# Kernel tuning notes

Measured on AMD Instinct MI355X. Metric: run time of the kernel, lower is better.

Reference implementation:

```python
import jax, jax.numpy as jnp
import numpy as np
from jax import lax

N_ITER = 50  # SparsemaxBisectFunction hardcodes n_iter=50


def _sparsemax_bisect(X):
    # alpha = 2: gp(x)=x, gp_inv(y)=y, p(x)=clamp(x, 0). X*(alpha-1) == X.
    d = X.shape[-1]
    max_val = jnp.max(X, axis=-1, keepdims=True)
    tau_lo = max_val - 1.0          # max - gp(1)
    tau_hi = max_val - 1.0 / d      # max - gp(1/d)
    f_lo = jnp.sum(jnp.maximum(X - tau_lo, 0.0), axis=-1) - 1.0
    dm = tau_hi - tau_lo

    def body(_, carry):
        tau_lo, dm, _tau_m = carry
        dm = dm * 0.5
        tau_m = tau_lo + dm
        f_m = jnp.sum(jnp.maximum(X - tau_m, 0.0), axis=-1) - 1.0
        mask = (f_m * f_lo >= 0.0)[..., None]
        tau_lo = jnp.where(mask, tau_m, tau_lo)
        return tau_lo, dm, tau_m

    _, _, tau_m = lax.fori_loop(0, N_ITER, body, (tau_lo, dm, tau_lo))
    p = jnp.maximum(X - tau_m, 0.0)  # p_m from the last bisection iteration
    p = p / jnp.sum(p, axis=-1, keepdims=True)  # ensure_sum_one=True
    return p


def setup_inputs() -> dict:
    key = jax.random.key(0)
    X = jax.random.normal(key, (4096, 32000), dtype=jnp.float32)
    return {"X": X}


def reference(X):
    return _sparsemax_bisect(X)
```

## Files before the change

### kernel.cpp

```cpp
#include <hip/hip_runtime.h>
#include <math.h>
#include <stdint.h>

constexpr int D = 32000;
constexpr int BLOCK = 1024;
constexpr int NW = BLOCK / 64;
constexpr int FULL4 = D / (4 * BLOCK);
constexpr int REM_THREADS = (D - FULL4 * 4 * BLOCK) / 4;
constexpr int NV = FULL4 + 1;
constexpr int CAP = 1024;
constexpr int NITER = 50;
constexpr int PERSIST = 256;

__device__ __forceinline__ float wave_sum(float s) {
#pragma unroll
  for (int o = 32; o > 0; o >>= 1) s += __shfl_xor(s, o, 64);
  return s;
}

__device__ __forceinline__ void bar_lds() {
  asm volatile("s_waitcnt lgkmcnt(0)" ::: "memory");
  __builtin_amdgcn_s_barrier();
  asm volatile("" ::: "memory");
}

typedef __attribute__((address_space(3))) void lds_void;
typedef const __attribute__((address_space(1))) void glb_void;

__device__ __forceinline__ void gload16(const float* g, float* l) {
  __builtin_amdgcn_global_load_lds((glb_void*)g, (lds_void*)l, 16, 0, 0);
}

__global__ __launch_bounds__(BLOCK, 4)
void sparsemax_bisect_kernel(const float* __restrict__ X,
                             float* __restrict__ Out,
                             int rows, int nblk) {
  __shared__ __attribute__((aligned(16))) float srow[D];
  __shared__ float s_cand[CAP];
  __shared__ float s_red[NW];
  __shared__ int s_cnt[2];

  const int t = threadIdx.x;
  const int lane = t & 63;
  const int wid = t >> 6;
  const bool has_rem = (t < REM_THREADS);

  if (t < 2) s_cnt[t] = 0;

  long r = blockIdx.x;

  {
    const float* Xr = X + r * (long)D;
#pragma unroll
    for (int j = 0; j < FULL4; ++j)
      gload16(Xr + 4 * (j * BLOCK + t), srow + 4 * (j * BLOCK + t));
    if (has_rem)
      gload16(Xr + 4 * (FULL4 * BLOCK + t), srow + 4 * (FULL4 * BLOCK + t));
  }
  asm volatile("s_waitcnt vmcnt(0) lgkmcnt(0)" ::: "memory");
  __builtin_amdgcn_s_barrier();
  asm volatile("" ::: "memory");

  int par = 0;
  for (;;) {
    const long rn = r + nblk;
    const bool pf = (rn < rows);

    float4 o[NV];
#pragma unroll
    for (int j = 0; j < FULL4; ++j)
      o[j] = *reinterpret_cast<const float4*>(srow + 4 * (j * BLOCK + t));
    o[FULL4] =
        has_rem
            ? *reinterpret_cast<const float4*>(srow + 4 * (FULL4 * BLOCK + t))
            : make_float4(-INFINITY, -INFINITY, -INFINITY, -INFINITY);
#pragma unroll
    for (int j = 0; j < NV; ++j)
      asm volatile("" : "+v"(o[j].x), "+v"(o[j].y), "+v"(o[j].z), "+v"(o[j].w));

    if (pf) {
      const float* Xn = X + rn * (long)D;
#pragma unroll
      for (int j = 0; j < FULL4; ++j)
        gload16(Xn + 4 * (j * BLOCK + t), srow + 4 * (j * BLOCK + t));
      if (has_rem)
        gload16(Xn + 4 * (FULL4 * BLOCK + t), srow + 4 * (FULL4 * BLOCK + t));
    }

    float m = -INFINITY;
#pragma unroll
    for (int j = 0; j < NV; ++j)
      m = fmaxf(m, fmaxf(fmaxf(o[j].x, o[j].y), fmaxf(o[j].z, o[j].w)));
#pragma unroll
    for (int off = 32; off > 0; off >>= 1) m = fmaxf(m, __shfl_xor(m, off, 64));
    if (lane == 0) s_red[wid] = m;
    bar_lds();
    float rowmax = s_red[0];
#pragma unroll
    for (int j = 1; j < NW; ++j) rowmax = fmaxf(rowmax, s_red[j]);

    const float thresh = rowmax - 1.0f;
#pragma unroll
    for (int j = 0; j < NV; ++j) {
      const float a0 = o[j].x, a1 = o[j].y, a2 = o[j].z, a3 = o[j].w;
      if (a0 > thresh) { int i = atomicAdd(&s_cnt[par], 1); if (i < CAP) s_cand[i] = a0; }
      if (a1 > thresh) { int i = atomicAdd(&s_cnt[par], 1); if (i < CAP) s_cand[i] = a1; }
      if (a2 > thresh) { int i = atomicAdd(&s_cnt[par], 1); if (i < CAP) s_cand[i] = a2; }
      if (a3 > thresh) { int i = atomicAdd(&s_cnt[par], 1); if (i < CAP) s_cand[i] = a3; }
    }
    bar_lds();
    const int n = s_cnt[par];
    if (t == 0) s_cnt[par ^ 1] = 0;

    float tau, inv;
    if (n <= 64) {
      const float c = (lane < n) ? s_cand[lane] : -INFINITY;
      float tau_lo = rowmax - 1.0f;
      const float tau_hi = rowmax - (1.0f / (float)D);
      float dm = tau_hi - tau_lo;
      const float f_lo = wave_sum(fmaxf(c - tau_lo, 0.0f)) - 1.0f;
      float tau_m = tau_lo;
      for (int it = 0; it < NITER; ++it) {
        dm *= 0.5f;
        tau_m = tau_lo + dm;
        const float f_m = wave_sum(fmaxf(c - tau_m, 0.0f)) - 1.0f;
        if (f_m * f_lo >= 0.0f) tau_lo = tau_m;
      }
      const float sp = wave_sum(fmaxf(c - tau_m, 0.0f));
      tau = tau_m;
      inv = 1.0f / sp;
    } else if (n <= CAP) {
      float tau_lo = rowmax - 1.0f;
      const float tau_hi = rowmax - (1.0f / (float)D);
      float dm = tau_hi - tau_lo;
      float s0 = 0.0f;
      for (int i = lane; i < n; i += 64) s0 += fmaxf(s_cand[i] - tau_lo, 0.0f);
      const float f_lo = wave_sum(s0) - 1.0f;
      float tau_m = tau_lo;
      for (int it = 0; it < NITER; ++it) {
        dm *= 0.5f;
        tau_m = tau_lo + dm;
        float fs = 0.0f;
        for (int i = lane; i < n; i += 64) fs += fmaxf(s_cand[i] - tau_m, 0.0f);
        const float f_m = wave_sum(fs) - 1.0f;
        if (f_m * f_lo >= 0.0f) tau_lo = tau_m;
      }
      float sp = 0.0f;
      for (int i = lane; i < n; i += 64) sp += fmaxf(s_cand[i] - tau_m, 0.0f);
      tau = tau_m;
      inv = 1.0f / wave_sum(sp);
    } else {
      float tau_lo = rowmax - 1.0f;
      const float tau_hi = rowmax - (1.0f / (float)D);
      float dm = tau_hi - tau_lo;
      auto block_fsum = [&](float tt) -> float {
        float s = 0.0f;
#pragma unroll
        for (int j = 0; j < NV; ++j) {
          s += fmaxf(o[j].x - tt, 0.0f);
          s += fmaxf(o[j].y - tt, 0.0f);
          s += fmaxf(o[j].z - tt, 0.0f);
          s += fmaxf(o[j].w - tt, 0.0f);
        }
        s = wave_sum(s);
        bar_lds();
        if (lane == 0) s_red[wid] = s;
        bar_lds();
        float tot = s_red[0];
#pragma unroll
        for (int j = 1; j < NW; ++j) tot += s_red[j];
        return tot;
      };
      const float f_lo = block_fsum(tau_lo) - 1.0f;
      float tau_m = tau_lo;
      for (int it = 0; it < NITER; ++it) {
        dm *= 0.5f;
        tau_m = tau_lo + dm;
        const float f_m = block_fsum(tau_m) - 1.0f;
        if (f_m * f_lo >= 0.0f) tau_lo = tau_m;
      }
      const float sp = block_fsum(tau_m);
      tau = tau_m;
      inv = 1.0f / sp;
    }

    float* Or = Out + r * (long)D;
#pragma unroll
    for (int j = 0; j < FULL4; ++j) {
      float4 o4;
      o4.x = fmaxf(o[j].x - tau, 0.0f) * inv;
      o4.y = fmaxf(o[j].y - tau, 0.0f) * inv;
      o4.z = fmaxf(o[j].z - tau, 0.0f) * inv;
      o4.w = fmaxf(o[j].w - tau, 0.0f) * inv;
      *reinterpret_cast<float4*>(Or + 4 * (j * BLOCK + t)) = o4;
    }
    if (has_rem) {
      float4 o4;
      o4.x = fmaxf(o[FULL4].x - tau, 0.0f) * inv;
      o4.y = fmaxf(o[FULL4].y - tau, 0.0f) * inv;
      o4.z = fmaxf(o[FULL4].z - tau, 0.0f) * inv;
      o4.w = fmaxf(o[FULL4].w - tau, 0.0f) * inv;
      *reinterpret_cast<float4*>(Or + 4 * (FULL4 * BLOCK + t)) = o4;
    }

    if (!pf) break;
    r = rn;
    par ^= 1;

    if (has_rem) {
      asm volatile("s_waitcnt vmcnt(8) lgkmcnt(0)" ::: "memory");
    } else {
      asm volatile("s_waitcnt vmcnt(7) lgkmcnt(0)" ::: "memory");
    }
    __builtin_amdgcn_s_barrier();
    asm volatile("" ::: "memory");
  }
}

extern "C" void kernel_launch(void* const* d_in, const int* in_sizes, int n_in,
                              void* d_out, int out_size, void* d_ws, size_t ws_size,
                              hipStream_t stream) {
  const float* X = (const float*)d_in[0];
  float* Out = (float*)d_out;
  const int rows = in_sizes[0] / D;
  const int nblk = rows < PERSIST ? rows : PERSIST;
  hipLaunchKernelGGL(sparsemax_bisect_kernel, dim3(nblk), dim3(BLOCK), 0, stream,
                     X, Out, rows, nblk);
}
```

Baseline: 954.0 us.

## Replace 50-step bisection with exact sort-based sparsemax threshold for small candidate sets

For rows with at most 64 candidates above max-1, the wave now bitonic-sorts the candidates with shuffles, builds a prefix sum, and finds the exact sparsemax threshold through a ballot. This replaces the 50 serial wave reductions of the bisection loop with a fixed, shorter shuffle sequence. The exact tau can differ slightly from the bisection result after 50 iterations, which may matter for tolerance. The change affects only per-row compute latency, while the kernel is likely bound by memory bandwidth.

```diff
diff --git a/kernel.cpp b/kernel.cpp
--- a/kernel.cpp
+++ b/kernel.cpp
@@ -114,20 +114,31 @@
 
     float tau, inv;
     if (n <= 64) {
-      const float c = (lane < n) ? s_cand[lane] : -INFINITY;
-      float tau_lo = rowmax - 1.0f;
-      const float tau_hi = rowmax - (1.0f / (float)D);
-      float dm = tau_hi - tau_lo;
-      const float f_lo = wave_sum(fmaxf(c - tau_lo, 0.0f)) - 1.0f;
-      float tau_m = tau_lo;
-      for (int it = 0; it < NITER; ++it) {
-        dm *= 0.5f;
-        tau_m = tau_lo + dm;
-        const float f_m = wave_sum(fmaxf(c - tau_m, 0.0f)) - 1.0f;
-        if (f_m * f_lo >= 0.0f) tau_lo = tau_m;
-      }
-      const float sp = wave_sum(fmaxf(c - tau_m, 0.0f));
-      tau = tau_m;
+      const float corig = (lane < n) ? s_cand[lane] : -INFINITY;
+      float c = corig;
+#pragma unroll
+      for (int k = 2; k <= 64; k <<= 1) {
+#pragma unroll
+        for (int j = k >> 1; j > 0; j >>= 1) {
+          const float p = __shfl_xor(c, j, 64);
+          const bool low = (lane & j) == 0;
+          const bool asc = (lane & k) == 0;
+          const float mn = fminf(c, p), mx = fmaxf(c, p);
+          c = (low == asc) ? mx : mn;
+        }
+      }
+      float P = (lane < n) ? c : 0.0f;
+#pragma unroll
+      for (int off = 1; off < 64; off <<= 1) {
+        const float u = __shfl_up(P, off, 64);
+        if (lane >= off) P += u;
+      }
+      const float tauj = (P - 1.0f) / (float)(lane + 1);
+      const bool valid = (lane < n) && (c > tauj);
+      const unsigned long long b = __ballot(valid);
+      const int kstar = 64 - __clzll(b);
+      tau = __shfl(tauj, kstar - 1, 64);
+      const float sp = wave_sum(fmaxf(corig - tau, 0.0f));
       inv = 1.0f / sp;
     } else if (n <= CAP) {
       float tau_lo = rowmax - 1.0f;
```

Measured after the change: 882.8 us. -7.5%, faster.
